# Optimization experiments

Measured on AMD Instinct MI355X. Metric: run time of the kernel, lower is better.

The kernel has to match this reference:

```python
import jax, jax.numpy as jnp
import numpy as np

B = 1
F, Hh, Ww = 2, 30, 52           # grid_sizes (frames, height, width); 30*52 = 1560 tokens/frame
L = F * Hh * Ww                  # 3120 tokens
DIM = 1536
NH = 12
HD = DIM // NH                   # 128
EPS = 1e-6
SCALE = 1.0 / np.sqrt(HD)


def _rope_angles():
    # Matches causal_rope_apply: head_dim/2 = 64 complex channels split 22/21/21 (t/h/w).
    c = HD // 2
    tc = c - 2 * (c // 3)
    hc = c // 3
    wc = c // 3
    def ax(n, dh):
        inv = 1.0 / np.power(10000.0, np.arange(dh) * 2.0 / (2 * dh))
        return np.outer(np.arange(n), inv)  # [n, dh]
    ft, fh, fw = ax(F, tc), ax(Hh, hc), ax(Ww, wc)
    ang = np.concatenate([
        np.broadcast_to(ft[:, None, None, :], (F, Hh, Ww, tc)),
        np.broadcast_to(fh[None, :, None, :], (F, Hh, Ww, hc)),
        np.broadcast_to(fw[None, None, :, :], (F, Hh, Ww, wc)),
    ], axis=-1).reshape(L, c)
    return jnp.asarray(np.cos(ang), jnp.float32), jnp.asarray(np.sin(ang), jnp.float32)


def setup_inputs() -> dict:
    key = jax.random.key(0)
    ks = jax.random.split(key, 8)
    s = 1.0 / np.sqrt(DIM)
    d = {
        'x':  jax.random.normal(ks[0], (B, L, DIM), jnp.float32),
        'wq': jax.random.normal(ks[1], (DIM, DIM), jnp.float32) * s,
        'wk': jax.random.normal(ks[2], (DIM, DIM), jnp.float32) * s,
        'wv': jax.random.normal(ks[3], (DIM, DIM), jnp.float32) * s,
        'wo': jax.random.normal(ks[4], (DIM, DIM), jnp.float32) * s,
        'bq': jax.random.normal(ks[5], (DIM,), jnp.float32) * 0.02,
        'bk': jax.random.normal(ks[6], (DIM,), jnp.float32) * 0.02,
        'bv': jax.random.normal(ks[7], (DIM,), jnp.float32) * 0.02,
        'bo': jnp.zeros((DIM,), jnp.float32),
        'gq': jnp.ones((DIM,), jnp.float32),   # RMSNorm gain for q
        'gk': jnp.ones((DIM,), jnp.float32),   # RMSNorm gain for k
    }
    cos, sin = _rope_angles()
    d['freqs_cos'] = cos   # [L, HD//2]
    d['freqs_sin'] = sin
    return d


def _rms(x, g):
    return x * jax.lax.rsqrt(jnp.mean(x * x, axis=-1, keepdims=True) + EPS) * g


def _rope(x, cos, sin):
    # x: [B, L, NH, HD]; complex pairs are (even, odd) consecutive channels
    xs = x.reshape(B, L, NH, HD // 2, 2)
    xr, xi = xs[..., 0], xs[..., 1]
    c = cos[None, :, None, :]
    s = sin[None, :, None, :]
    out = jnp.stack([xr * c - xi * s, xr * s + xi * c], axis=-1)
    return out.reshape(B, L, NH, HD)


def reference(x, wq, wk, wv, wo, bq, bk, bv, bo, gq, gk, freqs_cos, freqs_sin):
    q = _rms(x @ wq + bq, gq).reshape(B, L, NH, HD)
    k = _rms(x @ wk + bk, gk).reshape(B, L, NH, HD)
    v = (x @ wv + bv).reshape(B, L, NH, HD)
    q = _rope(q, freqs_cos, freqs_sin)
    k = _rope(k, freqs_cos, freqs_sin)
    # block-causal per frame: query in frame i attends to keys in frames <= i
    frame = jnp.arange(L) // (Hh * Ww)
    mask = frame[None, :] <= frame[:, None]                     # [Lq, Lk]
    scores = jnp.einsum('bihd,bjhd->bhij', q, k) * SCALE        # [B, NH, L, L]
    scores = jnp.where(mask[None, None], scores, jnp.finfo(scores.dtype).min)
    p = jax.nn.softmax(scores, axis=-1)
    out = jnp.einsum('bhij,bjhd->bihd', p, v).reshape(B, L, DIM)
    return out @ wo + bo
```

## Files before the change

kernel.cpp:

```cpp
#include <hip/hip_runtime.h>
#include <hip/hip_bf16.h>

#define L_SEQ 3120
#define LPAD  3200
#define DIMN  1536
#define FRAME 1560
#define NHH   12
#define HDIM  128

using bh8   = __attribute__((ext_vector_type(8))) short;
using bh4   = __attribute__((ext_vector_type(4))) short;
using f32x4 = __attribute__((ext_vector_type(4))) float;
typedef unsigned short u16;
typedef unsigned int   u32;

static __device__ __forceinline__ u16 f2bf(float f) {
  __hip_bfloat16 h = __float2bfloat16(f);
  return *reinterpret_cast<u16*>(&h);
}
static __device__ __forceinline__ void gld16(const u16* g, u16* l) {
  __builtin_amdgcn_global_load_lds((const __attribute__((address_space(1))) void*)g,
                                   (__attribute__((address_space(3))) void*)l, 16, 0, 0);
}

__global__ __launch_bounds__(256) void prep_x_kern(const float* __restrict__ x,
                                                   u16* __restrict__ xb) {
  int i = (blockIdx.x * 256 + threadIdx.x) * 8;
  bh8 o;
  if (i < L_SEQ * DIMN) {
    float4 a = *(const float4*)&x[i];
    float4 b = *(const float4*)&x[i + 4];
    o[0] = (short)f2bf(a.x); o[1] = (short)f2bf(a.y);
    o[2] = (short)f2bf(a.z); o[3] = (short)f2bf(a.w);
    o[4] = (short)f2bf(b.x); o[5] = (short)f2bf(b.y);
    o[6] = (short)f2bf(b.z); o[7] = (short)f2bf(b.w);
  } else {
    o = (bh8){0, 0, 0, 0, 0, 0, 0, 0};
  }
  *(bh8*)&xb[i] = o;
}

__global__ __launch_bounds__(256) void transpose_w_kern(const float* __restrict__ w0, const float* __restrict__ w1,
                                 const float* __restrict__ w2, const float* __restrict__ w3,
                                 u16* __restrict__ t0, u16* __restrict__ t1,
                                 u16* __restrict__ t2, u16* __restrict__ t3) {
  __shared__ float tile[32][33];
  const float* src; u16* dst;
  switch (blockIdx.z) {
    case 0:  src = w0; dst = t0; break;
    case 1:  src = w1; dst = t1; break;
    case 2:  src = w2; dst = t2; break;
    default: src = w3; dst = t3; break;
  }
  int k0 = blockIdx.x * 32, n0 = blockIdx.y * 32;
  int tx = threadIdx.x, ty = threadIdx.y;
  #pragma unroll
  for (int i = 0; i < 4; i++)
    tile[ty * 4 + i][tx] = src[(size_t)(k0 + ty * 4 + i) * DIMN + n0 + tx];
  __syncthreads();
  #pragma unroll
  for (int i = 0; i < 4; i++) {
    int ry = ty * 4 + i;
    dst[(size_t)(n0 + ry) * DIMN + k0 + tx] = f2bf(tile[tx][ry]);
  }
}

__global__ __launch_bounds__(256) void zero_tail_kern(u16* __restrict__ ob) {
  int i = (blockIdx.x * 256 + threadIdx.x) * 8;
  *(bh8*)&ob[L_SEQ * DIMN + i] = (bh8){0, 0, 0, 0, 0, 0, 0, 0};
}

__global__ __launch_bounds__(256) void gemm_qkv(const u16* __restrict__ A,
                                                const u16* __restrict__ Bt,
                                                const float* __restrict__ bq,
                                                const float* __restrict__ bk,
                                                const float* __restrict__ bv,
                                                float* __restrict__ lin,
                                                u16* __restrict__ Vt) {
  __shared__ __align__(16) u16 Al[128 * 64];
  __shared__ __align__(16) u16 Bl[128 * 64];
  int t = threadIdx.x, lane = t & 63, w = t >> 6;
  int m0 = blockIdx.x * 128, n0 = blockIdx.y * 128;
  int wr = (w >> 1) * 64, wc = (w & 1) * 64;
  int r16 = lane & 15, g8 = (lane >> 4) * 8;
  int lrow = lane >> 3, lcol = (lane & 7) * 8;
  f32x4 acc[4][4];
  #pragma unroll
  for (int i = 0; i < 4; i++)
    #pragma unroll
    for (int j = 0; j < 4; j++) acc[i][j] = (f32x4){0.f, 0.f, 0.f, 0.f};

  const u16* Abase = A + (size_t)(m0 + w * 32 + lrow) * DIMN + lcol;
  const u16* Bbase = Bt + (size_t)(n0 + w * 32 + lrow) * DIMN + lcol;

  for (int kt = 0; kt < DIMN; kt += 64) {
    __syncthreads();
    #pragma unroll
    for (int j = 0; j < 4; j++) {
      gld16(Abase + (size_t)j * 8 * DIMN + kt, &Al[(w * 32 + j * 8) * 64]);
      gld16(Bbase + (size_t)j * 8 * DIMN + kt, &Bl[(w * 32 + j * 8) * 64]);
    }
    __syncthreads();
    bh8 af[2][4], bf[2][4];
    #pragma unroll
    for (int kk = 0; kk < 2; kk++) {
      #pragma unroll
      for (int i = 0; i < 4; i++)
        af[kk][i] = *(const bh8*)&Al[(wr + i * 16 + r16) * 64 + kk * 32 + g8];
      #pragma unroll
      for (int j = 0; j < 4; j++)
        bf[kk][j] = *(const bh8*)&Bl[(wc + j * 16 + r16) * 64 + kk * 32 + g8];
    }
    #pragma unroll
    for (int kk = 0; kk < 2; kk++)
      #pragma unroll
      for (int i = 0; i < 4; i++)
        #pragma unroll
        for (int j = 0; j < 4; j++)
          acc[i][j] = __builtin_amdgcn_mfma_f32_16x16x32_bf16(af[kk][i], bf[kk][j], acc[i][j], 0, 0, 0);
  }

  int cr = (lane >> 4) * 4, cc = lane & 15;
  int seg = n0 / DIMN;
  int nb0 = n0 - seg * DIMN;
  const float* bp = (seg == 0) ? bq : (seg == 1) ? bk : bv;
  if (seg < 2) {
    #pragma unroll
    for (int j = 0; j < 4; j++) {
      int n = nb0 + wc + j * 16 + cc;
      float bvv = bp[n];
      #pragma unroll
      for (int i = 0; i < 4; i++) {
        int m = m0 + wr + i * 16 + cr;
        float* orow = lin + (size_t)m * (2 * DIMN) + seg * DIMN + n;
        #pragma unroll
        for (int r = 0; r < 4; r++) orow[(size_t)r * (2 * DIMN)] = acc[i][j][r] + bvv;
      }
    }
  } else {
    #pragma unroll
    for (int j = 0; j < 4; j++) {
      int d = nb0 + wc + j * 16 + cc;
      float bvv = bp[d];
      #pragma unroll
      for (int i = 0; i < 4; i++) {
        int m = m0 + wr + i * 16 + cr;
        if (m < L_SEQ) {
          bh4 o;
          #pragma unroll
          for (int r = 0; r < 4; r++) o[r] = (short)f2bf(acc[i][j][r] + bvv);
          *(bh4*)&Vt[(size_t)d * L_SEQ + m] = o;
        }
      }
    }
  }
}

__global__ __launch_bounds__(256) void gemm_out(const u16* __restrict__ A,
                                                const u16* __restrict__ Bt,
                                                const float* __restrict__ bias,
                                                float* __restrict__ out) {
  __shared__ __align__(16) u16 Al[128 * 64];
  __shared__ __align__(16) u16 Bl[128 * 64];
  int t = threadIdx.x, lane = t & 63, w = t >> 6;
  int m0 = blockIdx.x * 128, n0 = blockIdx.y * 128;
  int wr = (w >> 1) * 64, wc = (w & 1) * 64;
  int r16 = lane & 15, g8 = (lane >> 4) * 8;
  int lrow = lane >> 3, lcol = (lane & 7) * 8;
  f32x4 acc[4][4];
  #pragma unroll
  for (int i = 0; i < 4; i++)
    #pragma unroll
    for (int j = 0; j < 4; j++) acc[i][j] = (f32x4){0.f, 0.f, 0.f, 0.f};

  const u16* Abase = A + (size_t)(m0 + w * 32 + lrow) * DIMN + lcol;
  const u16* Bbase = Bt + (size_t)(n0 + w * 32 + lrow) * DIMN + lcol;

  for (int kt = 0; kt < DIMN; kt += 64) {
    __syncthreads();
    #pragma unroll
    for (int j = 0; j < 4; j++) {
      gld16(Abase + (size_t)j * 8 * DIMN + kt, &Al[(w * 32 + j * 8) * 64]);
      gld16(Bbase + (size_t)j * 8 * DIMN + kt, &Bl[(w * 32 + j * 8) * 64]);
    }
    __syncthreads();
    bh8 af[2][4], bf[2][4];
    #pragma unroll
    for (int kk = 0; kk < 2; kk++) {
      #pragma unroll
      for (int i = 0; i < 4; i++)
        af[kk][i] = *(const bh8*)&Al[(wr + i * 16 + r16) * 64 + kk * 32 + g8];
      #pragma unroll
      for (int j = 0; j < 4; j++)
        bf[kk][j] = *(const bh8*)&Bl[(wc + j * 16 + r16) * 64 + kk * 32 + g8];
    }
    #pragma unroll
    for (int kk = 0; kk < 2; kk++)
      #pragma unroll
      for (int i = 0; i < 4; i++)
        #pragma unroll
        for (int j = 0; j < 4; j++)
          acc[i][j] = __builtin_amdgcn_mfma_f32_16x16x32_bf16(af[kk][i], bf[kk][j], acc[i][j], 0, 0, 0);
  }

  int cr = (lane >> 4) * 4, cc = lane & 15;
  #pragma unroll
  for (int j = 0; j < 4; j++) {
    int n = n0 + wc + j * 16 + cc;
    float bvv = bias[n];
    #pragma unroll
    for (int i = 0; i < 4; i++) {
      int m = m0 + wr + i * 16 + cr;
      if (m < L_SEQ) {
        #pragma unroll
        for (int r = 0; r < 4; r++) out[(size_t)(m + r) * DIMN + n] = acc[i][j][r] + bvv;
      }
    }
  }
}

__global__ __launch_bounds__(256) void postproc_qk(const float* __restrict__ lin,
                                                   const float* __restrict__ gq,
                                                   const float* __restrict__ gk,
                                                   const float* __restrict__ fc,
                                                   const float* __restrict__ fs,
                                                   u16* __restrict__ Qb, u16* __restrict__ Kb) {
  int l = blockIdx.x, t = threadIdx.x;
  int lane = t & 63, w = t >> 6;
  const float2* qr = (const float2*)(lin + (size_t)l * (2 * DIMN));
  const float2* kr = qr + DIMN / 2;
  float2 qv[3], kv[3];
  float ssq = 0.f, ssk = 0.f;
  #pragma unroll
  for (int j = 0; j < 3; j++) {
    qv[j] = qr[t + j * 256];
    kv[j] = kr[t + j * 256];
    ssq += qv[j].x * qv[j].x + qv[j].y * qv[j].y;
    ssk += kv[j].x * kv[j].x + kv[j].y * kv[j].y;
  }
  __shared__ float red[8];
  #pragma unroll
  for (int off = 32; off; off >>= 1) {
    ssq += __shfl_xor(ssq, off);
    ssk += __shfl_xor(ssk, off);
  }
  if (lane == 0) { red[w] = ssq; red[4 + w] = ssk; }
  __syncthreads();
  float rrq = rsqrtf((red[0] + red[1] + red[2] + red[3]) * (1.0f / DIMN) + 1e-6f);
  float rrk = rsqrtf((red[4] + red[5] + red[6] + red[7]) * (1.0f / DIMN) + 1e-6f);
  u32* qo = (u32*)Qb;
  u32* ko = (u32*)Kb;
  #pragma unroll
  for (int j = 0; j < 3; j++) {
    int p = t + j * 256;
    int head = p >> 6, c = p & 63;
    float co = fc[l * 64 + c], si = fs[l * 64 + c];
    float2 g2, o;
    size_t idx = ((size_t)head * L_SEQ + l) * 64 + c;
    g2 = ((const float2*)gq)[p];
    o.x = qv[j].x * rrq * g2.x; o.y = qv[j].y * rrq * g2.y;
    qo[idx] = (u32)f2bf(o.x * co - o.y * si) | ((u32)f2bf(o.x * si + o.y * co) << 16);
    g2 = ((const float2*)gk)[p];
    o.x = kv[j].x * rrk * g2.x; o.y = kv[j].y * rrk * g2.y;
    ko[idx] = (u32)f2bf(o.x * co - o.y * si) | ((u32)f2bf(o.x * si + o.y * co) << 16);
  }
}

__global__ __launch_bounds__(256) void attn_kern(const u16* __restrict__ Q,
                                                 const u16* __restrict__ K,
                                                 const u16* __restrict__ Vt,
                                                 u16* __restrict__ Ob) {
  __shared__ __align__(16) u16 Kl[64][136];
  __shared__ __align__(16) u16 Vl[128][72];
  __shared__ __align__(16) u16 Pl[4][16][72];
  int t = threadIdx.x, lane = t & 63, w = t >> 6;
  int h = blockIdx.y, qb = blockIdx.x * 64, qr0 = qb + w * 16;
  int r16 = lane & 15, g8 = (lane >> 4) * 8;
  int cr = (lane >> 4) * 4, cc = lane & 15;
  const float sl = 0.08838834764831845f * 1.4426950408889634f;

  int qld = qr0 + r16; if (qld > L_SEQ - 1) qld = L_SEQ - 1;
  const u16* qrow = Q + ((size_t)h * L_SEQ + qld) * HDIM;
  bh8 qf[4];
  #pragma unroll
  for (int kk = 0; kk < 4; kk++) qf[kk] = *(const bh8*)&qrow[kk * 32 + g8];

  const u16* Kbase = K + (size_t)h * L_SEQ * HDIM;
  const u16* Vbase = Vt + (size_t)h * HDIM * L_SEQ;

  float m_run[4] = {-3.0e38f, -3.0e38f, -3.0e38f, -3.0e38f};
  float l_part[4] = {0.f, 0.f, 0.f, 0.f};
  f32x4 accO[8];
  #pragma unroll
  for (int i = 0; i < 8; i++) accO[i] = (f32x4){0.f, 0.f, 0.f, 0.f};

  int klim_min = (qr0 < FRAME) ? FRAME : L_SEQ;
  int klimr[4];
  #pragma unroll
  for (int r = 0; r < 4; r++) klimr[r] = (qr0 + cr + r < FRAME) ? FRAME : L_SEQ;

  int klimB = (qb + 63 < FRAME) ? FRAME : L_SEQ;
  int nkt = (klimB + 63) >> 6;

  for (int it = 0; it < nkt; ++it) {
    int kt = it << 6;
    __syncthreads();
    if (kt + 64 <= L_SEQ) {
      #pragma unroll
      for (int i = 0; i < 4; i++) {
        int e = t + i * 256;
        int krw = e >> 4, kc2 = (e & 15) * 8;
        *(bh8*)&Kl[krw][kc2] = *(const bh8*)&Kbase[(size_t)(kt + krw) * HDIM + kc2];
        int vd = e >> 3, vc = (e & 7) * 8;
        *(bh8*)&Vl[vd][vc] = *(const bh8*)&Vbase[(size_t)vd * L_SEQ + kt + vc];
      }
    } else {
      #pragma unroll
      for (int i = 0; i < 4; i++) {
        int e = t + i * 256;
        int krw = e >> 4, kc2 = (e & 15) * 8;
        int ks = kt + krw; if (ks > L_SEQ - 1) ks = L_SEQ - 1;
        *(bh8*)&Kl[krw][kc2] = *(const bh8*)&Kbase[(size_t)ks * HDIM + kc2];
        int vd = e >> 3, vc = (e & 7) * 8;
        int jb = kt + vc; if (jb > L_SEQ - 8) jb = L_SEQ - 8;
        *(bh8*)&Vl[vd][vc] = *(const bh8*)&Vbase[(size_t)vd * L_SEQ + jb];
      }
    }
    __syncthreads();

    f32x4 s[4];
    #pragma unroll
    for (int sb = 0; sb < 4; sb++) s[sb] = (f32x4){0.f, 0.f, 0.f, 0.f};
    #pragma unroll
    for (int kk = 0; kk < 4; kk++)
      #pragma unroll
      for (int sb = 0; sb < 4; sb++) {
        bh8 kf = *(const bh8*)&Kl[sb * 16 + r16][kk * 32 + g8];
        s[sb] = __builtin_amdgcn_mfma_f32_16x16x32_bf16(qf[kk], kf, s[sb], 0, 0, 0);
      }

    float v[4][4];
    if (kt + 64 > klim_min) {
      #pragma unroll
      for (int sb = 0; sb < 4; sb++) {
        int j = kt + sb * 16 + cc;
        #pragma unroll
        for (int r = 0; r < 4; r++) v[sb][r] = (j < klimr[r]) ? s[sb][r] * sl : -3.0e38f;
      }
    } else {
      #pragma unroll
      for (int sb = 0; sb < 4; sb++)
        #pragma unroll
        for (int r = 0; r < 4; r++) v[sb][r] = s[sb][r] * sl;
    }

    float loc[4];
    #pragma unroll
    for (int r = 0; r < 4; r++)
      loc[r] = fmaxf(fmaxf(v[0][r], v[1][r]), fmaxf(v[2][r], v[3][r]));
    bool need = (loc[0] > m_run[0] + 8.f) || (loc[1] > m_run[1] + 8.f) ||
                (loc[2] > m_run[2] + 8.f) || (loc[3] > m_run[3] + 8.f);
    if (__any((int)need)) {
      float facs[4];
      #pragma unroll
      for (int r = 0; r < 4; r++) {
        float mx = loc[r];
        mx = fmaxf(mx, __shfl_xor(mx, 1));
        mx = fmaxf(mx, __shfl_xor(mx, 2));
        mx = fmaxf(mx, __shfl_xor(mx, 4));
        mx = fmaxf(mx, __shfl_xor(mx, 8));
        float mnew = fmaxf(m_run[r], mx);
        facs[r] = exp2f(m_run[r] - mnew);
        m_run[r] = mnew;
        l_part[r] *= facs[r];
      }
      #pragma unroll
      for (int nb = 0; nb < 8; nb++)
        #pragma unroll
        for (int r = 0; r < 4; r++) accO[nb][r] *= facs[r];
    }
    #pragma unroll
    for (int sb = 0; sb < 4; sb++)
      #pragma unroll
      for (int r = 0; r < 4; r++) {
        float p = exp2f(v[sb][r] - m_run[r]);
        l_part[r] += p;
        Pl[w][cr + r][sb * 16 + cc] = f2bf(p);
      }

    bh8 pf0 = *(const bh8*)&Pl[w][r16][g8];
    bh8 pf1 = *(const bh8*)&Pl[w][r16][32 + g8];
    #pragma unroll
    for (int nb = 0; nb < 8; nb++) {
      bh8 vf0 = *(const bh8*)&Vl[nb * 16 + r16][g8];
      bh8 vf1 = *(const bh8*)&Vl[nb * 16 + r16][32 + g8];
      accO[nb] = __builtin_amdgcn_mfma_f32_16x16x32_bf16(pf0, vf0, accO[nb], 0, 0, 0);
      accO[nb] = __builtin_amdgcn_mfma_f32_16x16x32_bf16(pf1, vf1, accO[nb], 0, 0, 0);
    }
  }

  #pragma unroll
  for (int r = 0; r < 4; r++) {
    float lr = l_part[r];
    lr += __shfl_xor(lr, 1);
    lr += __shfl_xor(lr, 2);
    lr += __shfl_xor(lr, 4);
    lr += __shfl_xor(lr, 8);
    l_part[r] = 1.0f / lr;
  }
  #pragma unroll
  for (int nb = 0; nb < 8; nb++)
    #pragma unroll
    for (int r = 0; r < 4; r++) {
      int qi = qr0 + cr + r;
      if (qi < L_SEQ)
        Ob[(size_t)qi * DIMN + h * HDIM + nb * 16 + cc] = f2bf(accO[nb][r] * l_part[r]);
    }
}

extern "C" void kernel_launch(void* const* d_in, const int* in_sizes, int n_in,
                              void* d_out, int out_size, void* d_ws, size_t ws_size,
                              hipStream_t stream) {
  const float* x  = (const float*)d_in[0];
  const float* wq = (const float*)d_in[1];
  const float* wk = (const float*)d_in[2];
  const float* wv = (const float*)d_in[3];
  const float* wo = (const float*)d_in[4];
  const float* bq = (const float*)d_in[5];
  const float* bk = (const float*)d_in[6];
  const float* bv = (const float*)d_in[7];
  const float* bo = (const float*)d_in[8];
  const float* gq = (const float*)d_in[9];
  const float* gk = (const float*)d_in[10];
  const float* fc = (const float*)d_in[11];
  const float* fs = (const float*)d_in[12];

  char* ws = (char*)d_ws;
  u16* xb   = (u16*)(ws);
  u16* Btq  = (u16*)(ws + 9830400);
  u16* wot  = (u16*)(ws + 23986176);
  u16* Qb   = (u16*)(ws + 28704768);
  u16* Kb   = (u16*)(ws + 38289408);
  u16* Vt   = (u16*)(ws + 47874048);
  u16* Ob   = (u16*)(ws + 57458688);
  float* lin = (float*)(ws + 67289088);

  prep_x_kern<<<2400, 256, 0, stream>>>(x, xb);
  transpose_w_kern<<<dim3(48, 48, 4), dim3(32, 8), 0, stream>>>(
      wq, wk, wv, wo, Btq, Btq + DIMN * DIMN, Btq + 2 * DIMN * DIMN, wot);
  zero_tail_kern<<<60, 256, 0, stream>>>(Ob);

  gemm_qkv<<<dim3(25, 36), 256, 0, stream>>>(xb, Btq, bq, bk, bv, lin, Vt);
  postproc_qk<<<L_SEQ, 256, 0, stream>>>(lin, gq, gk, fc, fs, Qb, Kb);
  attn_kern<<<dim3(49, 12), 256, 0, stream>>>(Qb, Kb, Vt, Ob);
  gemm_out<<<dim3(25, 12), 256, 0, stream>>>(Ob, wot, bo, (float*)d_out);
}
```

Measured before the change: 403.4 us.

## Double-buffer K/V tiles with async global-to-LDS loads and XOR swizzle

The attention kernel now stages K and V tiles into double-buffered LDS with global_load_lds, so the next tile's load is issued before the current tile is computed. This hides global memory latency behind the MFMA work. It replaces padded LDS rows with an XOR swizzle to avoid bank conflicts, and reverses the block order so the heavier second-frame query blocks are scheduled first. LDS use rises, and correctness depends on the manual vmcnt counts and barriers.

```diff
diff --git a/kernel.cpp b/kernel.cpp
--- a/kernel.cpp
+++ b/kernel.cpp
@@ -270,13 +270,15 @@
                                                  const u16* __restrict__ K,
                                                  const u16* __restrict__ Vt,
                                                  u16* __restrict__ Ob) {
-  __shared__ __align__(16) u16 Kl[64][136];
-  __shared__ __align__(16) u16 Vl[128][72];
-  __shared__ __align__(16) u16 Pl[4][16][72];
+  __shared__ __align__(16) u16 KlB[2][64 * 128];
+  __shared__ __align__(16) u16 VlB[2][128 * 64];
+  __shared__ __align__(16) u16 Pl[4][16 * 72];
   int t = threadIdx.x, lane = t & 63, w = t >> 6;
-  int h = blockIdx.y, qb = blockIdx.x * 64, qr0 = qb + w * 16;
-  int r16 = lane & 15, g8 = (lane >> 4) * 8;
-  int cr = (lane >> 4) * 4, cc = lane & 15;
+  int h = blockIdx.y;
+  int bx = 48 - blockIdx.x;
+  int qb = bx * 64, qr0 = qb + w * 16;
+  int r16 = lane & 15, grp = lane >> 4, g8 = grp * 8;
+  int cr = grp * 4, cc = lane & 15;
   const float sl = 0.08838834764831845f * 1.4426950408889634f;
 
   int qld = qr0 + r16; if (qld > L_SEQ - 1) qld = L_SEQ - 1;
@@ -298,35 +300,38 @@
   int klimr[4];
   #pragma unroll
   for (int r = 0; r < 4; r++) klimr[r] = (qr0 + cr + r < FRAME) ? FRAME : L_SEQ;
-
   int klimB = (qb + 63 < FRAME) ? FRAME : L_SEQ;
   int nkt = (klimB + 63) >> 6;
 
+  auto stage = [&](int buf, int it) {
+    int kt = it << 6;
+    #pragma unroll
+    for (int j = 0; j < 4; j++) {
+      int rr = w * 16 + j * 4 + (lane >> 4);
+      int grow = kt + rr; grow = (grow > L_SEQ - 1) ? L_SEQ - 1 : grow;
+      int gc = ((lane & 15) ^ (rr & 7)) * 8;
+      gld16(Kbase + (size_t)grow * HDIM + gc, &KlB[buf][(w * 16 + j * 4) * 128]);
+    }
+    #pragma unroll
+    for (int j = 0; j < 4; j++) {
+      int vr = w * 32 + j * 8 + (lane >> 3);
+      int gc = kt + ((lane & 7) ^ (vr & 7)) * 8;
+      gc = (gc > L_SEQ - 8) ? L_SEQ - 8 : gc;
+      gld16(Vbase + (size_t)vr * L_SEQ + gc, &VlB[buf][(w * 32 + j * 8) * 64]);
+    }
+  };
+
+  stage(0, 0);
   for (int it = 0; it < nkt; ++it) {
-    int kt = it << 6;
-    __syncthreads();
-    if (kt + 64 <= L_SEQ) {
-      #pragma unroll
-      for (int i = 0; i < 4; i++) {
-        int e = t + i * 256;
-        int krw = e >> 4, kc2 = (e & 15) * 8;
-        *(bh8*)&Kl[krw][kc2] = *(const bh8*)&Kbase[(size_t)(kt + krw) * HDIM + kc2];
-        int vd = e >> 3, vc = (e & 7) * 8;
-        *(bh8*)&Vl[vd][vc] = *(const bh8*)&Vbase[(size_t)vd * L_SEQ + kt + vc];
-      }
+    int buf = it & 1, kt = it << 6;
+    if (it + 1 < nkt) {
+      stage(buf ^ 1, it + 1);
+      asm volatile("s_waitcnt vmcnt(8)" ::: "memory");
     } else {
-      #pragma unroll
-      for (int i = 0; i < 4; i++) {
-        int e = t + i * 256;
-        int krw = e >> 4, kc2 = (e & 15) * 8;
-        int ks = kt + krw; if (ks > L_SEQ - 1) ks = L_SEQ - 1;
-        *(bh8*)&Kl[krw][kc2] = *(const bh8*)&Kbase[(size_t)ks * HDIM + kc2];
-        int vd = e >> 3, vc = (e & 7) * 8;
-        int jb = kt + vc; if (jb > L_SEQ - 8) jb = L_SEQ - 8;
-        *(bh8*)&Vl[vd][vc] = *(const bh8*)&Vbase[(size_t)vd * L_SEQ + jb];
-      }
-    }
-    __syncthreads();
+      asm volatile("s_waitcnt vmcnt(0)" ::: "memory");
+    }
+    __builtin_amdgcn_s_barrier();
+    __builtin_amdgcn_sched_barrier(0);
 
     f32x4 s[4];
     #pragma unroll
@@ -335,7 +340,8 @@
     for (int kk = 0; kk < 4; kk++)
       #pragma unroll
       for (int sb = 0; sb < 4; sb++) {
-        bh8 kf = *(const bh8*)&Kl[sb * 16 + r16][kk * 32 + g8];
+        int rr = sb * 16 + r16;
+        bh8 kf = *(const bh8*)&KlB[buf][rr * 128 + (((kk * 4 + grp) ^ (rr & 7)) * 8)];
         s[sb] = __builtin_amdgcn_mfma_f32_16x16x32_bf16(qf[kk], kf, s[sb], 0, 0, 0);
       }
 
@@ -385,18 +391,20 @@
       for (int r = 0; r < 4; r++) {
         float p = exp2f(v[sb][r] - m_run[r]);
         l_part[r] += p;
-        Pl[w][cr + r][sb * 16 + cc] = f2bf(p);
-      }
-
-    bh8 pf0 = *(const bh8*)&Pl[w][r16][g8];
-    bh8 pf1 = *(const bh8*)&Pl[w][r16][32 + g8];
+        Pl[w][(cr + r) * 72 + sb * 16 + cc] = f2bf(p);
+      }
+
+    bh8 pf0 = *(const bh8*)&Pl[w][r16 * 72 + g8];
+    bh8 pf1 = *(const bh8*)&Pl[w][r16 * 72 + 32 + g8];
     #pragma unroll
     for (int nb = 0; nb < 8; nb++) {
-      bh8 vf0 = *(const bh8*)&Vl[nb * 16 + r16][g8];
-      bh8 vf1 = *(const bh8*)&Vl[nb * 16 + r16][32 + g8];
+      int vrow = nb * 16 + r16;
+      bh8 vf0 = *(const bh8*)&VlB[buf][vrow * 64 + ((grp ^ (vrow & 7)) * 8)];
+      bh8 vf1 = *(const bh8*)&VlB[buf][vrow * 64 + (((4 + grp) ^ (vrow & 7)) * 8)];
       accO[nb] = __builtin_amdgcn_mfma_f32_16x16x32_bf16(pf0, vf0, accO[nb], 0, 0, 0);
       accO[nb] = __builtin_amdgcn_mfma_f32_16x16x32_bf16(pf1, vf1, accO[nb], 0, 0, 0);
     }
+    __builtin_amdgcn_s_barrier();
   }
 
   #pragma unroll
```

New measurement: 398.2 us. Within noise of the previous version (-1.3%).
